# Optimization experiments

Hardware: AMD Instinct MI355X
Metric: run time of the kernel (lower is better)

The kernel has to match this reference:

```python
import jax, jax.numpy as jnp
import numpy as np

C = 512
NC = 12
EPS = 1e-5

ADJ = np.array([
    [0,0,0,1,0,1,1,1,1,1,1,1],
    [0,0,0,1,0,1,1,1,1,1,1,1],
    [0,0,0,1,0,1,1,1,1,1,1,1],
    [1,1,1,0,1,1,1,1,1,1,1,1],
    [0,0,0,1,0,1,1,1,1,1,1,1],
    [1,1,1,1,1,0,1,1,1,0,0,0],
    [1,1,1,1,1,1,0,0,0,1,1,1],
    [1,1,1,1,1,1,0,0,0,1,1,1],
    [1,1,1,1,1,1,0,0,0,1,1,1],
    [1,1,1,1,1,0,1,1,1,0,0,0],
    [1,1,1,1,1,0,1,1,1,0,0,0],
    [1,1,1,1,1,0,1,1,1,0,0,0]], dtype=np.float32)
# per-AU region selection: 0=up,1=mid,2=down1,3=down2 (AU1,2,4 up; AU6 mid; AU7 up; AU10 d2; AU12,14,15 d1; AU17,23,24 d2)
SEL = np.array([0,0,0,1,0,3,2,2,2,3,3,3])


def setup_inputs() -> dict:
    key = jax.random.key(0)
    ks = jax.random.split(key, 12)
    B, T = 32, 32
    BT = B * T
    s = (2.0 / C) ** 0.5
    return {
        'x': jax.random.normal(ks[0], (BT, 49, C), jnp.float32),
        'adj_mask': jnp.ones((BT, NC, NC), jnp.float32),
        'region_W': jax.random.normal(ks[1], (4, C, C), jnp.float32) * s,
        'region_b': jnp.zeros((4, C), jnp.float32),
        'region_gamma': jnp.ones((4, C), jnp.float32),
        'region_beta': jnp.zeros((4, C), jnp.float32),
        'upfc_W': jax.random.normal(ks[2], (C, 16), jnp.float32) * 0.02,
        'upfc_b': jnp.zeros((16,), jnp.float32),
        'midfc_W': jax.random.normal(ks[3], (C, 2), jnp.float32) * 0.02,
        'midfc_b': jnp.zeros((2,), jnp.float32),
        'd1fc_W': jax.random.normal(ks[4], (C, 8), jnp.float32) * 0.02,
        'd1fc_b': jnp.zeros((8,), jnp.float32),
        'd2fc_W': jax.random.normal(ks[5], (C, 16), jnp.float32) * 0.02,
        'd2fc_b': jnp.zeros((16,), jnp.float32),
        'class_W': jax.random.normal(ks[6], (NC, C, C), jnp.float32) * s,
        'class_b': jnp.zeros((NC, C), jnp.float32),
        'class_gamma': jnp.ones((NC, C), jnp.float32),
        'class_beta': jnp.zeros((NC, C), jnp.float32),
        'gat_W': jax.random.normal(ks[7], (C, C), jnp.float32) * 0.02,
        'gat_al': jax.random.normal(ks[8], (C,), jnp.float32) * 0.02,
        'gat_ar': jax.random.normal(ks[9], (C,), jnp.float32) * 0.02,
        'tconv_W': jax.random.normal(ks[10], (NC, C, 5), jnp.float32) * 0.1,
        'tconv_b': jnp.zeros((NC, C), jnp.float32),
        'tbn_gamma': jnp.ones((NC,), jnp.float32),
        'tbn_beta': jnp.zeros((NC,), jnp.float32),
        'B': B,
        'T': T,
    }


def _bn(x, gamma, beta, axes):
    # training-mode batch norm: stats over `axes`, affine per remaining channel
    mean = x.mean(axes, keepdims=True)
    var = x.var(axes, keepdims=True)
    return gamma * (x - mean) * jax.lax.rsqrt(var + EPS) + beta


def reference(x, adj_mask, region_W, region_b, region_gamma, region_beta,
              upfc_W, upfc_b, midfc_W, midfc_b, d1fc_W, d1fc_b, d2fc_W, d2fc_b,
              class_W, class_b, class_gamma, class_beta,
              gat_W, gat_al, gat_ar, tconv_W, tconv_b, tbn_gamma, tbn_beta, B, T):
    BT = x.shape[0]
    xg = x.reshape(BT, 7, 7, C)
    x_up = xg[:, :3].reshape(BT, 21, C)
    x_mid = xg[:, 2:5].reshape(BT, 21, C)
    x_down = xg[:, 4:].reshape(BT, 21, C)
    # 4 region LinearBlocks (fc -> BN over (batch,seq) per channel -> relu), batched
    regions = jnp.stack([x_up, x_mid, x_down, x_down])  # [4,BT,21,C]
    h = jnp.einsum('rbsc,rcd->rbsd', regions, region_W) + region_b[:, None, None, :]
    h = jax.nn.relu(_bn(h, region_gamma[:, None, None, :], region_beta[:, None, None, :], (1, 2)))
    up_pred = h[0].mean(1) @ upfc_W + upfc_b
    mid_pred = h[1].mean(1) @ midfc_W + midfc_b
    d1_pred = h[2].mean(1) @ d1fc_W + d1fc_b
    d2_pred = h[3].mean(1) @ d2fc_W + d2fc_b
    # 12 per-AU LinearBlocks, batched over the class dim
    cls_in = h[jnp.asarray(SEL)]  # [12,BT,21,C]
    y = jnp.einsum('nbsc,ncd->nbsd', cls_in, class_W) + class_b[:, None, None, :]
    y = jax.nn.relu(_bn(y, class_gamma[:, None, None, :], class_beta[:, None, None, :], (1, 2)))
    f_v = y.mean(2).transpose(1, 0, 2)  # [BT,12,C]
    # cross-region single-head GAT over the fixed 12-node graph, residual, thred=0.1
    adj = jnp.asarray(ADJ)[None] * adj_mask + jnp.eye(NC, dtype=x.dtype)
    hg = f_v @ gat_W  # [BT,12,C]
    e = jax.nn.leaky_relu((hg @ gat_al)[:, :, None] + (hg @ gat_ar)[:, None, :], 0.2)
    attn = jax.nn.softmax(jnp.where(adj > 0.1, e, -1e9), axis=-1)
    g = jnp.einsum('bij,bjc->bic', attn, hg) + f_v
    # per-class depthwise temporal Conv1d (k=5, pad=2, groups=C), batched over classes
    x4 = g.reshape(B, T, NC, C)
    xp = jnp.pad(x4, ((0, 0), (2, 2), (0, 0), (0, 0)))
    v = sum(xp[:, k:k + T] * tconv_W[None, None, :, :, k] for k in range(5)) + tconv_b[None, None]
    v = v.reshape(BT, NC, C)
    out = jax.nn.relu(_bn(v, tbn_gamma[None, :, None], tbn_beta[None, :, None], (0, 2)))
    return (up_pred, mid_pred, d1_pred, d2_pred, out)
```

## Files before the change

### kernel.cpp

```cpp
#include <hip/hip_runtime.h>
#include <hip/hip_bf16.h>

typedef unsigned short u16;
typedef __attribute__((ext_vector_type(8))) __bf16 bf16x8;
typedef __attribute__((ext_vector_type(8))) u16 u16x8;
typedef __attribute__((ext_vector_type(4))) float floatx4;

#define C_     512
#define NC_    12
#define BT_    1024
#define SEQ_   21
#define M_REG  21504
#define M_GAT  12288

__device__ __forceinline__ float bf2f(u16 u) {
  unsigned int v = ((unsigned int)u) << 16;
  float f; __builtin_memcpy(&f, &v, 4); return f;
}
__device__ __forceinline__ u16 f2bf(float f) {
  unsigned int b; __builtin_memcpy(&b, &f, 4);
  unsigned int r = (b + 0x7FFFu + ((b >> 16) & 1u)) >> 16;
  return (u16)r;
}
__device__ __forceinline__ float ldf(const void* p, size_t i, int f32) {
  return f32 ? ((const float*)p)[i] : bf2f(((const u16*)p)[i]);
}
__device__ __forceinline__ u16 ldbf(const void* p, size_t i, int f32) {
  return f32 ? f2bf(((const float*)p)[i]) : ((const u16*)p)[i];
}
__device__ __forceinline__ void stout(void* p, size_t i, float v, int f32) {
  if (f32) ((float*)p)[i] = v; else ((u16*)p)[i] = f2bf(v);
}

typedef __attribute__((address_space(1))) unsigned int as1_u32;
typedef __attribute__((address_space(3))) unsigned int as3_u32;
__device__ __forceinline__ void gl2lds16(const void* g, void* l) {
  __builtin_amdgcn_global_load_lds((const as1_u32*)g, (as3_u32*)l, 16, 0, 0);
}

__global__ void sent_k(float* __restrict__ o, float val) {
  const int i = blockIdx.x * 256 + threadIdx.x;
  if (i < 16384) o[i] = val;
}

__global__ void detect_k(const u16* __restrict__ x, int* __restrict__ flag) {
  __shared__ int cnt;
  if (threadIdx.x == 0) cnt = 0;
  __syncthreads();
  int bad = 0;
  for (int i = threadIdx.x; i < 4096; i += 256) {
    const float v = bf2f(x[i]);
    const float a = fabsf(v);
    if (!(a <= 1e4f)) bad++;
    else if (a > 0.f && a < 1e-35f) bad++;
  }
  atomicAdd(&cnt, bad);
  __syncthreads();
  if (threadIdx.x == 0) *flag = (cnt > 400) ? 1 : 0;
}

__global__ void zero_stats(float* __restrict__ p, int n) {
  const int id = blockIdx.x * 256 + threadIdx.x;
  if (id < n) p[id] = 0.f;
}

__global__ void transpose512(const void* __restrict__ rW, const void* __restrict__ cW,
                             const void* __restrict__ gW, u16* __restrict__ oR,
                             u16* __restrict__ oC, u16* __restrict__ oG,
                             const int* __restrict__ flagp) {
  const int f32 = *flagp;
  const int z = blockIdx.z;
  const void* src; u16* dst; size_t sofs = 0;
  if (z < 4)       { src = rW; sofs = (size_t)z*262144;     dst = oR + (size_t)z*262144; }
  else if (z < 16) { src = cW; sofs = (size_t)(z-4)*262144; dst = oC + (size_t)(z-4)*262144; }
  else             { src = gW;                              dst = oG; }
  __shared__ u16 t[32][33];
  const int tx = threadIdx.x;
  const int cy = blockIdx.y * 32, dx = blockIdx.x * 32;
  for (int i = threadIdx.y; i < 32; i += 8)
    t[i][tx] = ldbf(src, sofs + (size_t)(cy + i)*512 + dx + tx, f32);
  __syncthreads();
  for (int i = threadIdx.y; i < 32; i += 8)
    dst[(size_t)(dx + i)*512 + cy + tx] = t[tx][i];
}

template<int MODE>
__global__ __launch_bounds__(256)
void gemm_k(const void* __restrict__ Abase, const u16* __restrict__ Wtb,
            const void* __restrict__ biasb, u16* __restrict__ outb,
            float* __restrict__ ssumb, float* __restrict__ ssqb,
            const int* __restrict__ flagp, int pk, int n0)
{
  const int f32 = *flagp;
  const int z = blockIdx.z;
  const int zeff = (MODE == 1) ? (n0 + z) : z;
  const void* A = Abase;
  if (MODE == 1) A = (const void*)((const u16*)Abase +
        (size_t)((pk >> (zeff * 2)) & 3) * ((size_t)M_REG * C_));
  const u16* Wt = Wtb + (size_t)zeff * C_ * C_;
  u16* Out = outb + (size_t)z * (size_t)M_REG * C_;

  __shared__ __align__(16) u16 smem[64 * 132];
  u16* As = smem;
  u16* Bs = smem + 4096;

  const int tid  = threadIdx.x;
  const int w    = tid >> 6;
  const int lane = tid & 63;
  const int wm   = w >> 1, wn = w & 1;
  const int r16  = lane & 15, q = lane >> 4;

  const int band = (MODE == 2) ? 12 : 21;
  const int lin  = blockIdx.x;
  const int xcd  = lin & 7;
  const int idx  = lin >> 3;
  const int mi   = xcd * band + idx % band;
  const int ni   = idx / band;
  const int m0   = mi * 128;
  const int nn0  = ni * 128;

  const int sub = lane >> 2;
  const int kq  = (lane & 3) * 8;
  const int am0 = m0 + w*32 + sub;
  const int am1 = am0 + 16;
  long ga0, ga1;
  if (MODE == 0) {
    const int roff = (pk >> (z * 8)) & 0xFF;
    int q21 = am0 / 21; int rm = am0 - q21*21;
    ga0 = (long)q21*49 + roff + rm;
    q21 = am1 / 21; rm = am1 - q21*21;
    ga1 = (long)q21*49 + roff + rm;
  } else { ga0 = am0; ga1 = am1; }
  const size_t aOff0 = (size_t)ga0 * C_ + kq;
  const size_t aOff1 = (size_t)ga1 * C_ + kq;
  const u16* bSrc0 = Wt + (size_t)(nn0 + w*32 + sub) * C_ + kq;
  const u16* bSrc1 = bSrc0 + (size_t)16 * C_;
  u16* aDstW0 = &As[(w*32 +  0) * 32];
  u16* aDstW1 = &As[(w*32 + 16) * 32];
  u16* bDstW0 = &Bs[(w*32 +  0) * 32];
  u16* bDstW1 = &Bs[(w*32 + 16) * 32];
  u16x8* aLds0 = (u16x8*)&As[(w*32 + sub +  0) * 32 + kq];
  u16x8* aLds1 = (u16x8*)&As[(w*32 + sub + 16) * 32 + kq];

  floatx4 acc[4][4];
  #pragma unroll
  for (int i = 0; i < 4; i++)
    #pragma unroll
    for (int j = 0; j < 4; j++)
      acc[i][j] = (floatx4){0.f, 0.f, 0.f, 0.f};

  for (int kk = 0; kk < C_; kk += 32) {
    if (MODE == 0 && f32) {
      const float* p0 = (const float*)A + aOff0 + kk;
      const float* p1 = (const float*)A + aOff1 + kk;
      const floatx4 f00 = *(const floatx4*)p0;
      const floatx4 f01 = *(const floatx4*)(p0 + 4);
      const floatx4 f10 = *(const floatx4*)p1;
      const floatx4 f11 = *(const floatx4*)(p1 + 4);
      u16x8 va0, va1;
      #pragma unroll
      for (int j = 0; j < 4; j++) {
        va0[j] = f2bf(f00[j]); va0[4+j] = f2bf(f01[j]);
        va1[j] = f2bf(f10[j]); va1[4+j] = f2bf(f11[j]);
      }
      __syncthreads();
      gl2lds16(bSrc0, bDstW0); gl2lds16(bSrc1, bDstW1);
      *aLds0 = va0; *aLds1 = va1;
      __syncthreads();
    } else {
      __syncthreads();
      gl2lds16((const u16*)A + aOff0 + kk, aDstW0);
      gl2lds16((const u16*)A + aOff1 + kk, aDstW1);
      gl2lds16(bSrc0, bDstW0);
      gl2lds16(bSrc1, bDstW1);
      __syncthreads();
    }
    bSrc0 += 32; bSrc1 += 32;
    bf16x8 av[4], bv[4];
    #pragma unroll
    for (int mt = 0; mt < 4; mt++)
      av[mt] = *(const bf16x8*)&As[(wm*64 + mt*16 + r16)*32 + q*8];
    #pragma unroll
    for (int nt = 0; nt < 4; nt++)
      bv[nt] = *(const bf16x8*)&Bs[(wn*64 + nt*16 + r16)*32 + q*8];
    #pragma unroll
    for (int mt = 0; mt < 4; mt++)
      #pragma unroll
      for (int nt = 0; nt < 4; nt++)
        acc[mt][nt] = __builtin_amdgcn_mfma_f32_16x16x32_bf16(av[mt], bv[nt], acc[mt][nt], 0, 0, 0);
  }

  #pragma unroll
  for (int rh = 0; rh < 2; rh++) {
    __syncthreads();
    if (wm == rh) {
      #pragma unroll
      for (int nt = 0; nt < 4; nt++) {
        const int lcol = wn*64 + nt*16 + r16;
        float bvv = 0.f;
        if (MODE != 2) bvv = ldf(biasb, (size_t)zeff * C_ + nn0 + lcol, f32);
        float s = 0.f, s2 = 0.f;
        #pragma unroll
        for (int mt = 0; mt < 4; mt++) {
          #pragma unroll
          for (int p = 0; p < 4; p++) {
            const float v = acc[mt][nt][p] + bvv;
            s += v; s2 += v*v;
            smem[(mt*16 + q*4 + p)*132 + lcol] = f2bf(v);
          }
        }
        if (MODE != 2) {
          s  += __shfl_xor(s, 16);  s  += __shfl_xor(s, 32);
          s2 += __shfl_xor(s2, 16); s2 += __shfl_xor(s2, 32);
          if (q == 0) {
            atomicAdd(&ssumb[(size_t)zeff * C_ + nn0 + lcol], s);
            atomicAdd(&ssqb [(size_t)zeff * C_ + nn0 + lcol], s2);
          }
        }
      }
    }
    __syncthreads();
    #pragma unroll
    for (int rr = 0; rr < 4; rr++) {
      const int rl = rr*16 + (tid >> 4);
      const int cc = (tid & 15) * 8;
      const u16x8 vv = *(const u16x8*)&smem[rl*132 + cc];
      u16x8* dst = (u16x8*)&Out[(size_t)(m0 + rh*64 + rl) * C_ + nn0 + cc];
      if (MODE == 1) __builtin_nontemporal_store(vv, dst);
      else           *dst = vv;
    }
  }
}

__global__ void bn_region(u16* __restrict__ h, float* __restrict__ hbar,
                          const void* __restrict__ gamma, const void* __restrict__ beta,
                          const float* __restrict__ rsum, const float* __restrict__ rsq,
                          const int* __restrict__ flagp) {
  const int f32 = *flagp;
  const int gid  = blockIdx.x;
  const int r    = gid >> 8;
  const int bt   = ((gid & 255) << 2) + (threadIdx.x >> 6);
  const int lane = threadIdx.x & 63;
  const int d0   = lane * 8;
  const int rd   = r*512 + d0;
  float sc[8], sh[8], accv[8];
  #pragma unroll
  for (int j = 0; j < 8; j++) {
    const float mean = rsum[rd+j] * (1.f/21504.f);
    const float var  = fmaxf(rsq[rd+j] * (1.f/21504.f) - mean*mean, 0.f);
    sc[j] = ldf(gamma, rd+j, f32) * rsqrtf(var + 1e-5f);
    sh[j] = ldf(beta,  rd+j, f32) - mean * sc[j];
    accv[j] = 0.f;
  }
  const size_t base = ((size_t)r * M_REG + (size_t)bt * SEQ_) * C_ + d0;
  #pragma unroll
  for (int s = 0; s < SEQ_; s++) {
    u16x8 vv = *(u16x8*)&h[base + (size_t)s*C_];
    #pragma unroll
    for (int j = 0; j < 8; j++) {
      float v = fmaxf(sc[j] * bf2f(vv[j]) + sh[j], 0.f);
      vv[j] = f2bf(v);
      accv[j] += v;
    }
    *(u16x8*)&h[base + (size_t)s*C_] = vv;
  }
  float* hb = &hbar[((size_t)r * BT_ + bt) * C_ + d0];
  #pragma unroll
  for (int j = 0; j < 8; j++) hb[j] = accv[j] * (1.f/21.f);
}

__global__ void preds_k(const float* __restrict__ hbar,
                        const void* __restrict__ upW,  const void* __restrict__ upB,
                        const void* __restrict__ midW, const void* __restrict__ midB,
                        const void* __restrict__ d1W,  const void* __restrict__ d1B,
                        const void* __restrict__ d2W,  const void* __restrict__ d2B,
                        void* __restrict__ dout, const int* __restrict__ flagp) {
  const int f32 = *flagp;
  const int bt = blockIdx.x;
  __shared__ float hl[4][512];
  for (int i = threadIdx.x; i < 2048; i += 256)
    hl[i >> 9][i & 511] = hbar[((size_t)(i >> 9) * BT_ + bt) * C_ + (i & 511)];
  __syncthreads();
  const int j = threadIdx.x;
  if (j < 42) {
    int r, wdt, col; const void *W, *Bv; size_t oofs;
    if (j < 16)      { r=0; W=upW;  Bv=upB;  wdt=16; col=j;    oofs = (size_t)bt*16 + col; }
    else if (j < 18) { r=1; W=midW; Bv=midB; wdt=2;  col=j-16; oofs = 16384 + (size_t)bt*2 + col; }
    else if (j < 26) { r=2; W=d1W;  Bv=d1B;  wdt=8;  col=j-18; oofs = 18432 + (size_t)bt*8 + col; }
    else             { r=3; W=d2W;  Bv=d2B;  wdt=16; col=j-26; oofs = 26624 + (size_t)bt*16 + col; }
    float acc = ldf(Bv, col, f32);
    for (int d = 0; d < 512; d++) acc += hl[r][d] * ldf(W, d*wdt + col, f32);
    stout(dout, oofs, acc, f32);
  }
}

__global__ void bn_class_mean(const u16* __restrict__ ypre, u16* __restrict__ fv,
                              const void* __restrict__ gamma, const void* __restrict__ beta,
                              const float* __restrict__ csum, const float* __restrict__ csq,
                              const int* __restrict__ flagp, int n0) {
  const int f32 = *flagp;
  const int gid  = blockIdx.x;
  const int zz   = gid >> 8;
  const int bt   = ((gid & 255) << 2) + (threadIdx.x >> 6);
  const int lane = threadIdx.x & 63;
  const int d0   = lane * 8;
  const int n    = n0 + zz;
  const int nd   = n*512 + d0;
  float sc[8], sh[8], accv[8];
  #pragma unroll
  for (int j = 0; j < 8; j++) {
    const float mean = csum[nd+j] * (1.f/21504.f);
    const float var  = fmaxf(csq[nd+j] * (1.f/21504.f) - mean*mean, 0.f);
    sc[j] = ldf(gamma, nd+j, f32) * rsqrtf(var + 1e-5f);
    sh[j] = ldf(beta,  nd+j, f32) - mean * sc[j];
    accv[j] = 0.f;
  }
  const size_t base = ((size_t)zz * M_REG + (size_t)bt * SEQ_) * C_ + d0;
  #pragma unroll
  for (int s = 0; s < SEQ_; s++) {
    const u16x8 vv = __builtin_nontemporal_load((const u16x8*)&ypre[base + (size_t)s*C_]);
    #pragma unroll
    for (int j = 0; j < 8; j++)
      accv[j] += fmaxf(sc[j] * bf2f(vv[j]) + sh[j], 0.f);
  }
  u16x8 ov;
  #pragma unroll
  for (int j = 0; j < 8; j++) ov[j] = f2bf(accv[j] * (1.f/21.f));
  *(u16x8*)&fv[((size_t)bt * NC_ + n) * C_ + d0] = ov;
}

__global__ __launch_bounds__(256)
void gat_k(const u16* __restrict__ hg, const u16* __restrict__ fv,
           const void* __restrict__ al, const void* __restrict__ ar,
           const void* __restrict__ adj_mask, float* __restrict__ g,
           const int* __restrict__ flagp) {
  const int f32 = *flagp;
  const int bt = blockIdx.x;
  __shared__ float hl[12][512];
  __shared__ float alv[12], arv[12], attn[12][12];
  const u16* hgb = hg + (size_t)bt * NC_ * C_;
  for (int i = threadIdx.x; i < 6144; i += 256)
    hl[i >> 9][i & 511] = bf2f(hgb[i]);
  __syncthreads();
  const int w = threadIdx.x >> 6, lane = threadIdx.x & 63;
  for (int i = w; i < 12; i += 4) {
    float pa = 0.f, pr = 0.f;
    #pragma unroll
    for (int jj = 0; jj < 8; jj++) {
      const int c = lane*8 + jj;
      const float hv = hl[i][c];
      pa += hv * ldf(al, c, f32);
      pr += hv * ldf(ar, c, f32);
    }
    #pragma unroll
    for (int off = 32; off; off >>= 1) { pa += __shfl_xor(pa, off); pr += __shfl_xor(pr, off); }
    if (lane == 0) { alv[i] = pa; arv[i] = pr; }
  }
  __syncthreads();
  if (threadIdx.x < 12) {
    const unsigned AM[12] = {0xFE8,0xFE8,0xFE8,0xFF7,0xFE8,0x1DF,
                             0xE3F,0xE3F,0xE3F,0x1DF,0x1DF,0x1DF};
    const int i = threadIdx.x;
    float row[12]; float mx = -1e30f;
    #pragma unroll
    for (int jx = 0; jx < 12; jx++) {
      const float maskv = ldf(adj_mask, (size_t)bt*144 + i*12 + jx, f32);
      const float adjv = (float)((AM[i] >> jx) & 1u) * maskv + (i == jx ? 1.f : 0.f);
      float e;
      if (adjv > 0.1f) {
        const float t = alv[i] + arv[jx];
        e = t > 0.f ? t : 0.2f * t;
      } else e = -1e9f;
      row[jx] = e; mx = fmaxf(mx, e);
    }
    float den = 0.f;
    #pragma unroll
    for (int jx = 0; jx < 12; jx++) { const float ex = __expf(row[jx] - mx); row[jx] = ex; den += ex; }
    const float inv = 1.f / den;
    #pragma unroll
    for (int jx = 0; jx < 12; jx++) attn[i][jx] = row[jx] * inv;
  }
  __syncthreads();
  const u16* fvb = fv + (size_t)bt * NC_ * C_;
  float* gb = g + (size_t)bt * NC_ * C_;
  for (int o = threadIdx.x; o < 6144; o += 256) {
    const int i = o >> 9, c = o & 511;
    float acc = bf2f(fvb[o]);
    #pragma unroll
    for (int jx = 0; jx < 12; jx++) acc += attn[i][jx] * hl[jx][c];
    gb[o] = acc;
  }
}

__global__ void tconv_k(float* __restrict__ g, const void* __restrict__ tw,
                        const void* __restrict__ tb, float* __restrict__ tsum,
                        float* __restrict__ tsq, const int* __restrict__ flagp) {
  const int f32 = *flagp;
  const int id = blockIdx.x * 256 + threadIdx.x;
  const int c = id & 511;
  const int n = (id >> 9) % 12;
  const int b = id / 6144;
  float wk[5];
  #pragma unroll
  for (int k = 0; k < 5; k++) wk[k] = ldf(tw, (size_t)(n*512 + c)*5 + k, f32);
  const float bias = ldf(tb, n*512 + c, f32);
  float xv[36];
  xv[0] = xv[1] = xv[34] = xv[35] = 0.f;
  const size_t base = ((size_t)b * 32 * NC_ + n) * C_ + c;
  #pragma unroll
  for (int t = 0; t < 32; t++) xv[t + 2] = g[base + (size_t)t * 6144];
  float s = 0.f, s2 = 0.f;
  float ov[32];
  #pragma unroll
  for (int t = 0; t < 32; t++) {
    float v = bias;
    #pragma unroll
    for (int k = 0; k < 5; k++) v += wk[k] * xv[t + k];
    ov[t] = v; s += v; s2 += v*v;
  }
  #pragma unroll
  for (int t = 0; t < 32; t++) g[base + (size_t)t * 6144] = ov[t];
  #pragma unroll
  for (int off = 32; off; off >>= 1) { s += __shfl_xor(s, off); s2 += __shfl_xor(s2, off); }
  if ((threadIdx.x & 63) == 0) { atomicAdd(&tsum[n], s); atomicAdd(&tsq[n], s2); }
}

__global__ void bn_t(const float* __restrict__ v, void* __restrict__ outp,
                     const void* __restrict__ tg, const void* __restrict__ tb2,
                     const float* __restrict__ tsum, const float* __restrict__ tsq,
                     const int* __restrict__ flagp) {
  const int f32 = *flagp;
  const size_t id = (size_t)blockIdx.x * 256 + threadIdx.x;
  const int n = (int)((id >> 9) % 12);
  const float mean = tsum[n] * (1.f/524288.f);
  const float var  = fmaxf(tsq[n] * (1.f/524288.f) - mean*mean, 0.f);
  const float sc = ldf(tg, n, f32) * rsqrtf(var + 1e-5f);
  const float sh = ldf(tb2, n, f32) - mean * sc;
  stout(outp, 43008 + id, fmaxf(sc * v[id] + sh, 0.f), f32);
}

static constexpr size_t OFF_FLAG = 0;
static constexpr size_t OFF_STAT = 64;
static constexpr int    STAT_N   = 2048+2048+6144+6144+12+12;
static constexpr size_t OFF_WTR  = 65792;
static constexpr size_t OFF_WTC  = OFF_WTR + (size_t)4*512*512*2;
static constexpr size_t OFF_WTG  = OFF_WTC + (size_t)12*512*512*2;
static constexpr size_t OFF_H    = OFF_WTG + (size_t)512*512*2;
static constexpr size_t OFF_HBAR = OFF_H + (size_t)4*M_REG*C_*2;
static constexpr size_t OFF_FV   = OFF_HBAR + (size_t)4*BT_*C_*4;
static constexpr size_t OFF_AREN = OFF_FV + (size_t)M_GAT*C_*2;
static constexpr size_t YPRE_B   = (size_t)M_REG * C_ * 2;
static constexpr size_t NEEDED   = OFF_AREN + YPRE_B;

extern "C" void kernel_launch(void* const* d_in, const int* in_sizes, int n_in,
                              void* d_out, int out_size, void* d_ws, size_t ws_size,
                              hipStream_t stream) {
  const u16* x        = (const u16*)d_in[0];
  const void* adj_m   = d_in[1];
  const void* region_W= d_in[2];
  const void* region_b= d_in[3];
  const void* region_g= d_in[4];
  const void* region_be=d_in[5];
  const void* upW  = d_in[6];   const void* upB  = d_in[7];
  const void* midW = d_in[8];   const void* midB = d_in[9];
  const void* d1W  = d_in[10];  const void* d1B  = d_in[11];
  const void* d2W  = d_in[12];  const void* d2B  = d_in[13];
  const void* class_W = d_in[14];
  const void* class_b = d_in[15];
  const void* class_g = d_in[16];
  const void* class_be= d_in[17];
  const void* gat_W   = d_in[18];
  const void* gat_al  = d_in[19];
  const void* gat_ar  = d_in[20];
  const void* tconv_W = d_in[21];
  const void* tconv_b = d_in[22];
  const void* tbn_g   = d_in[23];
  const void* tbn_be  = d_in[24];

  char* ws = (char*)d_ws;
  int*   flagp = (int*)(ws + OFF_FLAG);
  float* rsum = (float*)(ws + OFF_STAT);
  float* rsq  = rsum + 2048;
  float* csum = rsq  + 2048;
  float* csq  = csum + 6144;
  float* tsum = csq  + 6144;
  float* tsq  = tsum + 12;
  u16*   WtR  = (u16*)(ws + OFF_WTR);
  u16*   WtC  = (u16*)(ws + OFF_WTC);
  u16*   WtG  = (u16*)(ws + OFF_WTG);
  u16*   h    = (u16*)(ws + OFF_H);
  float* hbar = (float*)(ws + OFF_HBAR);
  u16*   fv   = (u16*)(ws + OFF_FV);
  u16*   ypre = (u16*)(ws + OFF_AREN);
  u16*   hg   = (u16*)(ws + OFF_AREN);
  float* g    = (float*)(ws + OFF_H);

  int errStage = 0, errCode = 0;
  (void)hipGetLastError();
  #define CK(s) do { hipError_t e_ = hipGetLastError(); \
      if (e_ != hipSuccess && errStage == 0) { errStage = (s); errCode = (int)e_; } } while(0)

  sent_k<<<64, 256, 0, stream>>>((float*)d_out, 50.f); CK(12);

  if (ws_size < NEEDED) {
    int mb = (int)(ws_size >> 20); if (mb > 999) mb = 999;
    sent_k<<<64, 256, 0, stream>>>((float*)d_out, 13000.f + (float)mb);
    return;
  }

  int nch = (int)((ws_size - OFF_AREN) / YPRE_B);
  if (nch > 12) nch = 12;
  if (nch < 1) nch = 1;

  const int ROFFPACK = 0 | (14 << 8) | (28 << 16) | (28 << 24);
  const int SELPACK  = (1 << 6) | (3 << 10) | (2 << 12) | (2 << 14) |
                       (2 << 16) | (3 << 18) | (3 << 20) | (3 << 22);

  detect_k<<<1, 256, 0, stream>>>(x, flagp);                         CK(1);
  zero_stats<<<(STAT_N + 255)/256, 256, 0, stream>>>(rsum, STAT_N);  CK(1);
  transpose512<<<dim3(16,16,17), dim3(32,8), 0, stream>>>(
      region_W, class_W, gat_W, WtR, WtC, WtG, flagp);               CK(2);

  gemm_k<0><<<dim3(672,1,4), 256, 0, stream>>>(
      x, WtR, region_b, h, rsum, rsq, flagp, ROFFPACK, 0);           CK(3);
  bn_region<<<1024, 256, 0, stream>>>(h, hbar, region_g, region_be,
      rsum, rsq, flagp);                                             CK(4);
  preds_k<<<1024, 256, 0, stream>>>(hbar, upW,upB, midW,midB,
      d1W,d1B, d2W,d2B, d_out, flagp);                               CK(5);

  for (int n0 = 0; n0 < 12; n0 += nch) {
    const int zc = (12 - n0) < nch ? (12 - n0) : nch;
    gemm_k<1><<<dim3(672,1,zc), 256, 0, stream>>>(
        h, WtC, class_b, ypre, csum, csq, flagp, SELPACK, n0);       CK(6);
    bn_class_mean<<<zc*256, 256, 0, stream>>>(ypre, fv, class_g, class_be,
        csum, csq, flagp, n0);                                       CK(7);
  }

  gemm_k<2><<<dim3(384,1,1), 256, 0, stream>>>(
      fv, WtG, nullptr, hg, nullptr, nullptr, flagp, 0, 0);          CK(8);
  gat_k<<<1024, 256, 0, stream>>>(hg, fv, gat_al, gat_ar, adj_m, g, flagp); CK(9);
  tconv_k<<<768, 256, 0, stream>>>(g, tconv_W, tconv_b, tsum, tsq, flagp);  CK(10);
  bn_t<<<24576, 256, 0, stream>>>(g, d_out, tbn_g, tbn_be, tsum, tsq, flagp); CK(11);

  if (errStage) {
    int ec = errCode > 999 ? 999 : errCode;
    sent_k<<<64, 256, 0, stream>>>((float*)d_out, (float)(errStage*1000 + ec));
  }
  #undef CK
}
```

Before: 798.2 us.

## Double GEMM K-tile to 64 with k-chunk-major LDS layout

The bf16 MFMA GEMM now loads a 64-wide K slice per iteration instead of 32, halving the number of barrier pairs per output tile. Shared memory is reorganized into 8-element k-chunk-major planes (128 rows × 8 k per plane), so each lane's 16-byte fragment read for the MFMA comes from a contiguous conflict-free stride. Global-to-LDS loads are reassigned so each wave fills two k-chunks for all 128 rows. LDS use doubles to 32 KB, which may lower occupancy, and each thread issues more loads per iteration.

```diff
diff --git a/kernel.cpp b/kernel.cpp
--- a/kernel.cpp
+++ b/kernel.cpp
@@ -100,9 +100,9 @@
   const u16* Wt = Wtb + (size_t)zeff * C_ * C_;
   u16* Out = outb + (size_t)z * (size_t)M_REG * C_;
 
-  __shared__ __align__(16) u16 smem[64 * 132];
+  __shared__ __align__(16) u16 smem[16384];
   u16* As = smem;
-  u16* Bs = smem + 4096;
+  u16* Bs = smem + 8192;
 
   const int tid  = threadIdx.x;
   const int w    = tid >> 6;
@@ -119,28 +119,20 @@
   const int m0   = mi * 128;
   const int nn0  = ni * 128;
 
-  const int sub = lane >> 2;
-  const int kq  = (lane & 3) * 8;
-  const int am0 = m0 + w*32 + sub;
-  const int am1 = am0 + 16;
-  long ga0, ga1;
+  long gaE, gaO;
   if (MODE == 0) {
     const int roff = (pk >> (z * 8)) & 0xFF;
-    int q21 = am0 / 21; int rm = am0 - q21*21;
-    ga0 = (long)q21*49 + roff + rm;
-    q21 = am1 / 21; rm = am1 - q21*21;
-    ga1 = (long)q21*49 + roff + rm;
-  } else { ga0 = am0; ga1 = am1; }
-  const size_t aOff0 = (size_t)ga0 * C_ + kq;
-  const size_t aOff1 = (size_t)ga1 * C_ + kq;
-  const u16* bSrc0 = Wt + (size_t)(nn0 + w*32 + sub) * C_ + kq;
-  const u16* bSrc1 = bSrc0 + (size_t)16 * C_;
-  u16* aDstW0 = &As[(w*32 +  0) * 32];
-  u16* aDstW1 = &As[(w*32 + 16) * 32];
-  u16* bDstW0 = &Bs[(w*32 +  0) * 32];
-  u16* bDstW1 = &Bs[(w*32 + 16) * 32];
-  u16x8* aLds0 = (u16x8*)&As[(w*32 + sub +  0) * 32 + kq];
-  u16x8* aLds1 = (u16x8*)&As[(w*32 + sub + 16) * 32 + kq];
+    int r = m0 + lane;       int q21 = r / 21, rm = r - q21*21;
+    gaE = (long)q21*49 + roff + rm;
+    r = m0 + 64 + lane;      q21 = r / 21; rm = r - q21*21;
+    gaO = (long)q21*49 + roff + rm;
+  } else { gaE = m0 + lane; gaO = m0 + 64 + lane; }
+  const u16* aE = (const u16*)A + (size_t)gaE * C_ + w*16;
+  const u16* aO = (const u16*)A + (size_t)gaO * C_ + w*16;
+  const u16* bE = Wt + (size_t)(nn0 + lane) * C_ + w*16;
+  const u16* bO = bE + (size_t)64 * C_;
+  u16* aL = &As[w * 4 * 512];
+  u16* bL = &Bs[w * 4 * 512];
 
   floatx4 acc[4][4];
   #pragma unroll
@@ -149,45 +141,55 @@
     for (int j = 0; j < 4; j++)
       acc[i][j] = (floatx4){0.f, 0.f, 0.f, 0.f};
 
-  for (int kk = 0; kk < C_; kk += 32) {
+  for (int kk = 0; kk < C_; kk += 64) {
     if (MODE == 0 && f32) {
-      const float* p0 = (const float*)A + aOff0 + kk;
-      const float* p1 = (const float*)A + aOff1 + kk;
-      const floatx4 f00 = *(const floatx4*)p0;
-      const floatx4 f01 = *(const floatx4*)(p0 + 4);
-      const floatx4 f10 = *(const floatx4*)p1;
-      const floatx4 f11 = *(const floatx4*)(p1 + 4);
-      u16x8 va0, va1;
+      u16x8 va[4];
       #pragma unroll
       for (int j = 0; j < 4; j++) {
-        va0[j] = f2bf(f00[j]); va0[4+j] = f2bf(f01[j]);
-        va1[j] = f2bf(f10[j]); va1[4+j] = f2bf(f11[j]);
+        const long ga = (j & 1) ? gaO : gaE;
+        const float* p = (const float*)A + (size_t)ga * C_ + kk + w*16 + (j >> 1)*8;
+        const floatx4 f0 = *(const floatx4*)p;
+        const floatx4 f1 = *(const floatx4*)(p + 4);
+        #pragma unroll
+        for (int e = 0; e < 4; e++) { va[j][e] = f2bf(f0[e]); va[j][4+e] = f2bf(f1[e]); }
       }
       __syncthreads();
-      gl2lds16(bSrc0, bDstW0); gl2lds16(bSrc1, bDstW1);
-      *aLds0 = va0; *aLds1 = va1;
-      __syncthreads();
+      gl2lds16(bE,     bL);
+      gl2lds16(bO,     bL + 512);
+      gl2lds16(bE + 8, bL + 1024);
+      gl2lds16(bO + 8, bL + 1536);
+      #pragma unroll
+      for (int j = 0; j < 4; j++)
+        *(u16x8*)(aL + j*512 + lane*8) = va[j];
     } else {
       __syncthreads();
-      gl2lds16((const u16*)A + aOff0 + kk, aDstW0);
-      gl2lds16((const u16*)A + aOff1 + kk, aDstW1);
-      gl2lds16(bSrc0, bDstW0);
-      gl2lds16(bSrc1, bDstW1);
-      __syncthreads();
-    }
-    bSrc0 += 32; bSrc1 += 32;
-    bf16x8 av[4], bv[4];
-    #pragma unroll
-    for (int mt = 0; mt < 4; mt++)
-      av[mt] = *(const bf16x8*)&As[(wm*64 + mt*16 + r16)*32 + q*8];
-    #pragma unroll
-    for (int nt = 0; nt < 4; nt++)
-      bv[nt] = *(const bf16x8*)&Bs[(wn*64 + nt*16 + r16)*32 + q*8];
-    #pragma unroll
-    for (int mt = 0; mt < 4; mt++)
+      gl2lds16(aE,     aL);
+      gl2lds16(aO,     aL + 512);
+      gl2lds16(aE + 8, aL + 1024);
+      gl2lds16(aO + 8, aL + 1536);
+      gl2lds16(bE,     bL);
+      gl2lds16(bO,     bL + 512);
+      gl2lds16(bE + 8, bL + 1024);
+      gl2lds16(bO + 8, bL + 1536);
+    }
+    aE += 64; aO += 64; bE += 64; bO += 64;
+    __syncthreads();
+    #pragma unroll
+    for (int s = 0; s < 2; s++) {
+      const int kb = (s*4 + q) * 1024;
+      bf16x8 av[4], bv[4];
+      #pragma unroll
+      for (int mt = 0; mt < 4; mt++)
+        av[mt] = *(const bf16x8*)&As[kb + (wm*64 + mt*16 + r16)*8];
       #pragma unroll
       for (int nt = 0; nt < 4; nt++)
-        acc[mt][nt] = __builtin_amdgcn_mfma_f32_16x16x32_bf16(av[mt], bv[nt], acc[mt][nt], 0, 0, 0);
+        bv[nt] = *(const bf16x8*)&Bs[kb + (wn*64 + nt*16 + r16)*8];
+      #pragma unroll
+      for (int mt = 0; mt < 4; mt++)
+        #pragma unroll
+        for (int nt = 0; nt < 4; nt++)
+          acc[mt][nt] = __builtin_amdgcn_mfma_f32_16x16x32_bf16(av[mt], bv[nt], acc[mt][nt], 0, 0, 0);
+    }
   }
 
   #pragma unroll
```

Result: slower. 1.023 ms (+28.2%).
